# Kernel tuning notes

Measured on AMD Instinct MI355X. Metric: run time of the kernel, lower is better.

## Reference

```python
import jax, jax.numpy as jnp
import numpy as np

B, C, IN, OUT = 8192, 64, 64, 64


def setup_inputs() -> dict:
    key = jax.random.key(0)
    k1, k2, k3 = jax.random.split(key, 3)
    x = jax.random.normal(k1, (B, C, IN), dtype=jnp.float32)
    # kernel shape [1, category, in_channel, out_channel], bias [1, category, out_channel]
    kernel = jax.random.normal(k2, (1, C, IN, OUT), dtype=jnp.float32) * (1.0 / np.sqrt(IN))
    bias = jax.random.normal(k3, (1, C, OUT), dtype=jnp.float32) * 0.01
    return {"x": x, "kernel": kernel, "bias": bias}


def reference(x, kernel, bias):
    # Faithful to: sum(x[:,:,:,None] * kernel, dim=2) + bias, expressed as a
    # per-category batched GEMM to avoid the (B,C,IN,OUT) intermediate.
    out = jnp.einsum('bci,cio->bco', x, kernel[0])  # (B, C, OUT)
    out = out + bias  # bias broadcasts over batch
    # activation is None in this config
    return out
```

## Files before the change

### kernel.cpp

```cpp
#include <hip/hip_runtime.h>


constexpr int C_   = 64;
constexpr int IN_  = 64;
constexpr int OUT_ = 64;
constexpr int BT   = 256;

typedef __attribute__((ext_vector_type(8))) short bf16x8;
typedef __attribute__((ext_vector_type(4))) float f32x4;

typedef __attribute__((address_space(1))) const void gvoid_t;
typedef __attribute__((address_space(3))) void lvoid_t;

__device__ __forceinline__ void gl_lds16(const float* g, float* l) {
    __builtin_amdgcn_global_load_lds((gvoid_t*)g, (lvoid_t*)l, 16, 0, 0);
}

__device__ __forceinline__ short f2bf(float f) {
    union { float f; unsigned u; } v; v.f = f;
    unsigned r = v.u + 0x7FFF + ((v.u >> 16) & 1);
    return (short)(r >> 16);
}

__global__ __launch_bounds__(256)
void cat_dense_mfma(const float* __restrict__ x,
                    const float* __restrict__ k,
                    const float* __restrict__ bias,
                    float* __restrict__ out) {
    __shared__ float ksm[IN_ * OUT_];

    const int tid  = threadIdx.x;
    const int wv   = tid >> 6;
    const int lane = tid & 63;
    const int c    = blockIdx.x & 63;
    const long bBase = (long)(blockIdx.x >> 6) * BT;

    const int lrow = lane & 15;
    const int lkg  = lane >> 4;

    #pragma unroll
    for (int it = 0; it < 4; ++it) {
        int gb = wv * 256 + it * 64;
        gl_lds16(k + (size_t)c * (IN_ * OUT_) + (size_t)(gb + lane) * 4,
                 &ksm[gb * 4]);
    }

    bf16x8 af[8];
    #pragma unroll
    for (int p = 0; p < 2; ++p)
      #pragma unroll
      for (int mt = 0; mt < 2; ++mt)
        #pragma unroll
        for (int ksi = 0; ksi < 2; ++ksi) {
            const float* xp = x
                + (size_t)(bBase + wv * 64 + p * 32 + mt * 16 + lrow) * (C_ * IN_)
                + (size_t)c * IN_ + ksi * 32 + lkg * 8;
            f32x4 lo = *(const f32x4*)xp;
            f32x4 hi = *(const f32x4*)(xp + 4);
            bf16x8 a;
            #pragma unroll
            for (int e = 0; e < 4; ++e) {
                a[e]     = f2bf(lo[e]);
                a[4 + e] = f2bf(hi[e]);
            }
            af[(p * 2 + mt) * 2 + ksi] = a;
        }

    float bv[4];
    #pragma unroll
    for (int nt = 0; nt < 4; ++nt)
        bv[nt] = bias[(size_t)c * OUT_ + nt * 16 + lrow];

    __syncthreads();

    bf16x8 kb[4][2];
    #pragma unroll
    for (int nt = 0; nt < 4; ++nt)
      #pragma unroll
      for (int ksi = 0; ksi < 2; ++ksi) {
        bf16x8 b;
        #pragma unroll
        for (int j = 0; j < 8; ++j)
            b[j] = f2bf(ksm[(ksi * 32 + lkg * 8 + j) * OUT_ + nt * 16 + lrow]);
        kb[nt][ksi] = b;
      }

    #pragma unroll
    for (int p = 0; p < 2; ++p) {
        f32x4 acc[2][4];
        #pragma unroll
        for (int mt = 0; mt < 2; ++mt)
          #pragma unroll
          for (int nt = 0; nt < 4; ++nt)
            acc[mt][nt] = (f32x4){0.f, 0.f, 0.f, 0.f};

        #pragma unroll
        for (int ksi = 0; ksi < 2; ++ksi)
          #pragma unroll
          for (int mt = 0; mt < 2; ++mt) {
            bf16x8 a = af[(p * 2 + mt) * 2 + ksi];
            #pragma unroll
            for (int nt = 0; nt < 4; ++nt)
                acc[mt][nt] = __builtin_amdgcn_mfma_f32_16x16x32_bf16(
                                  a, kb[nt][ksi], acc[mt][nt], 0, 0, 0);
          }

        #pragma unroll
        for (int mt = 0; mt < 2; ++mt) {
            size_t rbase = (size_t)(bBase + wv * 64 + p * 32 + mt * 16 + lkg * 4)
                               * (C_ * OUT_)
                         + (size_t)c * OUT_ + lrow;
            #pragma unroll
            for (int reg = 0; reg < 4; ++reg)
              #pragma unroll
              for (int nt = 0; nt < 4; ++nt)
                __builtin_nontemporal_store(
                    acc[mt][nt][reg] + bv[nt],
                    out + rbase + (size_t)reg * (C_ * OUT_) + nt * 16);
        }
    }
}

extern "C" void kernel_launch(void* const* d_in, const int* in_sizes, int n_in,
                              void* d_out, int out_size, void* d_ws, size_t ws_size,
                              hipStream_t stream) {
    const float* x    = (const float*)d_in[0];
    const float* k    = (const float*)d_in[1];
    const float* bias = (const float*)d_in[2];
    float* out        = (float*)d_out;

    const int B     = in_sizes[0] / (C_ * IN_);
    const int tiles = B / BT;
    dim3 grid(64 * tiles);
    cat_dense_mfma<<<grid, 256, 0, stream>>>(x, k, bias, out);
}
```

Measured before the change: 54.03 us.

## Stage bf16 x tile in swizzled LDS and swap MFMA operands for vector stores

The x tile is now loaded cooperatively with coalesced float4 reads, converted to bf16, and stored in LDS with an XOR swizzle. Each wave then reads its A fragments back from LDS. The kernel weights are converted to bf16 once while being staged into LDS, and the MFMA operand order is swapped so the result is transposed. That lets each lane write 16-byte vector nontemporal stores along the output row instead of scalar strided stores. The cost is 32KB of extra LDS per block and an added LDS round trip, which may limit occupancy.

```diff
diff --git a/kernel.cpp b/kernel.cpp
--- a/kernel.cpp
+++ b/kernel.cpp
@@ -7,14 +7,8 @@
 constexpr int BT   = 256;
 
 typedef __attribute__((ext_vector_type(8))) short bf16x8;
+typedef __attribute__((ext_vector_type(4))) short s16x4;
 typedef __attribute__((ext_vector_type(4))) float f32x4;
-
-typedef __attribute__((address_space(1))) const void gvoid_t;
-typedef __attribute__((address_space(3))) void lvoid_t;
-
-__device__ __forceinline__ void gl_lds16(const float* g, float* l) {
-    __builtin_amdgcn_global_load_lds((gvoid_t*)g, (lvoid_t*)l, 16, 0, 0);
-}
 
 __device__ __forceinline__ short f2bf(float f) {
     union { float f; unsigned u; } v; v.f = f;
@@ -22,12 +16,13 @@
     return (short)(r >> 16);
 }
 
-__global__ __launch_bounds__(256)
-void cat_dense_mfma(const float* __restrict__ x,
-                    const float* __restrict__ k,
-                    const float* __restrict__ bias,
-                    float* __restrict__ out) {
-    __shared__ float ksm[IN_ * OUT_];
+__global__ __launch_bounds__(256, 4)
+void cat_dense_mfma2(const float* __restrict__ x,
+                     const float* __restrict__ k,
+                     const float* __restrict__ bias,
+                     float* __restrict__ out) {
+    __shared__ unsigned short xsb[BT * IN_];
+    __shared__ unsigned short ksb[IN_ * OUT_];
 
     const int tid  = threadIdx.x;
     const int wv   = tid >> 6;
@@ -40,36 +35,31 @@
 
     #pragma unroll
     for (int it = 0; it < 4; ++it) {
-        int gb = wv * 256 + it * 64;
-        gl_lds16(k + (size_t)c * (IN_ * OUT_) + (size_t)(gb + lane) * 4,
-                 &ksm[gb * 4]);
+        int p = tid + it * 256;
+        f32x4 v = *(const f32x4*)(k + (size_t)c * (IN_ * OUT_) + p * 4);
+        s16x4 w;
+        #pragma unroll
+        for (int e = 0; e < 4; ++e) w[e] = f2bf(v[e]);
+        *(s16x4*)(&ksb[p * 4]) = w;
     }
 
-    bf16x8 af[8];
     #pragma unroll
-    for (int p = 0; p < 2; ++p)
-      #pragma unroll
-      for (int mt = 0; mt < 2; ++mt)
+    for (int it = 0; it < 16; ++it) {
+        int q   = tid + it * 256;
+        int row = q >> 4, s8 = q & 15;
+        f32x4 v = *(const f32x4*)(x + (size_t)(bBase + row) * (C_ * IN_)
+                                    + c * IN_ + s8 * 4);
+        s16x4 w;
         #pragma unroll
-        for (int ksi = 0; ksi < 2; ++ksi) {
-            const float* xp = x
-                + (size_t)(bBase + wv * 64 + p * 32 + mt * 16 + lrow) * (C_ * IN_)
-                + (size_t)c * IN_ + ksi * 32 + lkg * 8;
-            f32x4 lo = *(const f32x4*)xp;
-            f32x4 hi = *(const f32x4*)(xp + 4);
-            bf16x8 a;
-            #pragma unroll
-            for (int e = 0; e < 4; ++e) {
-                a[e]     = f2bf(lo[e]);
-                a[4 + e] = f2bf(hi[e]);
-            }
-            af[(p * 2 + mt) * 2 + ksi] = a;
-        }
+        for (int e = 0; e < 4; ++e) w[e] = f2bf(v[e]);
+        int byteoff = row * 128 + ((((s8 >> 1) ^ (row & 7)) << 4) | ((s8 & 1) << 3));
+        *(s16x4*)((char*)xsb + byteoff) = w;
+    }
 
-    float bv[4];
+    f32x4 bv[4];
     #pragma unroll
     for (int nt = 0; nt < 4; ++nt)
-        bv[nt] = bias[(size_t)c * OUT_ + nt * 16 + lrow];
+        bv[nt] = *(const f32x4*)(bias + (size_t)c * OUT_ + nt * 16 + lkg * 4);
 
     __syncthreads();
 
@@ -81,12 +71,22 @@
         bf16x8 b;
         #pragma unroll
         for (int j = 0; j < 8; ++j)
-            b[j] = f2bf(ksm[(ksi * 32 + lkg * 8 + j) * OUT_ + nt * 16 + lrow]);
+            b[j] = (short)ksb[(ksi * 32 + lkg * 8 + j) * OUT_ + nt * 16 + lrow];
         kb[nt][ksi] = b;
       }
 
     #pragma unroll
     for (int p = 0; p < 2; ++p) {
+        bf16x8 af[2][2];
+        #pragma unroll
+        for (int mt = 0; mt < 2; ++mt)
+          #pragma unroll
+          for (int ksi = 0; ksi < 2; ++ksi) {
+            int row = wv * 64 + p * 32 + mt * 16 + lrow;
+            int byteoff = row * 128 + ((((ksi * 4 + lkg)) ^ (row & 7)) << 4);
+            af[mt][ksi] = *(const bf16x8*)((const char*)xsb + byteoff);
+          }
+
         f32x4 acc[2][4];
         #pragma unroll
         for (int mt = 0; mt < 2; ++mt)
@@ -97,26 +97,22 @@
         #pragma unroll
         for (int ksi = 0; ksi < 2; ++ksi)
           #pragma unroll
-          for (int mt = 0; mt < 2; ++mt) {
-            bf16x8 a = af[(p * 2 + mt) * 2 + ksi];
+          for (int mt = 0; mt < 2; ++mt)
             #pragma unroll
             for (int nt = 0; nt < 4; ++nt)
                 acc[mt][nt] = __builtin_amdgcn_mfma_f32_16x16x32_bf16(
-                                  a, kb[nt][ksi], acc[mt][nt], 0, 0, 0);
-          }
+                                  kb[nt][ksi], af[mt][ksi], acc[mt][nt], 0, 0, 0);
 
         #pragma unroll
         for (int mt = 0; mt < 2; ++mt) {
-            size_t rbase = (size_t)(bBase + wv * 64 + p * 32 + mt * 16 + lkg * 4)
+            size_t rbase = (size_t)(bBase + wv * 64 + p * 32 + mt * 16 + lrow)
                                * (C_ * OUT_)
-                         + (size_t)c * OUT_ + lrow;
+                         + (size_t)c * OUT_ + lkg * 4;
             #pragma unroll
-            for (int reg = 0; reg < 4; ++reg)
-              #pragma unroll
-              for (int nt = 0; nt < 4; ++nt)
-                __builtin_nontemporal_store(
-                    acc[mt][nt][reg] + bv[nt],
-                    out + rbase + (size_t)reg * (C_ * OUT_) + nt * 16);
+            for (int nt = 0; nt < 4; ++nt) {
+                f32x4 o = acc[mt][nt] + bv[nt];
+                __builtin_nontemporal_store(o, (f32x4*)(out + rbase + nt * 16));
+            }
         }
     }
 }
@@ -132,5 +128,5 @@
     const int B     = in_sizes[0] / (C_ * IN_);
     const int tiles = B / BT;
     dim3 grid(64 * tiles);
-    cat_dense_mfma<<<grid, 256, 0, stream>>>(x, k, bias, out);
+    cat_dense_mfma2<<<grid, 256, 0, stream>>>(x, k, bias, out);
 }
```

Result: no change. 54.96 us (+1.7%).
